# Performance work log

Hardware: AMD Instinct MI355X
Metric: run time of the kernel (lower is better)

## Reference

```python
import jax, jax.numpy as jnp
import numpy as np

TOP_K = 2
EPS = 1e-6

def setup_inputs() -> dict:
    key = jax.random.key(0)
    ks = jax.random.split(key, 6)
    Bt, S, D, E, R = 4, 4096, 1024, 8, 4
    s = lambda d: 1.0 / np.sqrt(d)
    return {
        "x": jax.random.normal(ks[0], (Bt, S, D), jnp.float32),
        "W_base": jax.random.normal(ks[1], (D, D), jnp.float32) * s(D),
        "b_base": jax.random.normal(ks[2], (D,), jnp.float32) * 0.02,
        "W_router": jax.random.normal(ks[3], (E, D), jnp.float32) * s(D),
        "A": jax.random.normal(ks[4], (E, D, R), jnp.float32) * s(D),
        "B": jax.random.normal(ks[5], (E, R, D), jnp.float32) * s(R),
    }

def reference(x, W_base, b_base, W_router, A, B):
    # frozen base linear: [b,s,d] @ [out,d]^T + bias
    base_out = jnp.einsum('bsd,od->bso', x, W_base) + b_base
    # router softmax gate over experts
    logits = jnp.einsum('bsd,ed->bse', x, W_router)
    gate = jax.nn.softmax(logits, axis=-1)
    # top-k scatter-mask (values kept are the gate values themselves)
    topv, topi = jax.lax.top_k(gate, TOP_K)                    # [b,s,k]
    mask = jnp.sum(jax.nn.one_hot(topi, gate.shape[-1], dtype=gate.dtype), axis=-2)
    gate = gate * mask
    gate = gate / (jnp.sum(gate, axis=-1, keepdims=True) + EPS)
    # batched rank-4 LoRA experts, gating applied in low-rank space
    h = jnp.einsum('bsd,edr->bser', x, A)                      # [b,s,E,r]
    hg = h * gate[..., None]                                   # weight before up-proj
    lora_out = jnp.einsum('bser,ero->bso', hg, B)
    return base_out + lora_out
```

## Files before the change

### kernel.cpp

```cpp
#include <hip/hip_runtime.h>
#include <cstdint>

typedef __attribute__((ext_vector_type(8))) short short8;
typedef __attribute__((ext_vector_type(4))) float f32x4;

__device__ inline unsigned short f2bf(float f){
  union { float f; uint32_t u; } v; v.f = f;
  uint32_t r = v.u + 0x7FFFu + ((v.u >> 16) & 1u);
  return (unsigned short)(r >> 16);
}

#define GLL(gp, lp) __builtin_amdgcn_global_load_lds(              \
    (const __attribute__((address_space(1))) void*)(gp),           \
    (__attribute__((address_space(3))) void*)(lp), 16, 0, 0)

__global__ __launch_bounds__(256) void kconv(const float* __restrict__ W,
                                             const float* __restrict__ A,
                                             const float* __restrict__ Bm,
                                             unsigned short* __restrict__ Wb,
                                             unsigned short* __restrict__ BTt,
                                             unsigned short* __restrict__ W2b){
  int i = blockIdx.x * 256 + threadIdx.x;
  Wb[i] = f2bf(W[i]);
  if (i < 32768){
    int o = i >> 5, c = i & 31;
    BTt[i] = f2bf(Bm[(size_t)c*1024 + o]);
    int n = i >> 10, d = i & 1023;
    W2b[i] = f2bf(A[(((size_t)(n>>2))*1024 + d)*4 + (n&3)]);
  }
}

__global__ __launch_bounds__(256) void kxl3(const float* __restrict__ x,
                                            const float* __restrict__ Wr,
                                            unsigned short* __restrict__ xb,
                                            float* __restrict__ gate){
  __shared__ float wr[8192];
  const int tid  = threadIdx.x;
  {
    const float4* s  = (const float4*)Wr;
    float4*       d4 = (float4*)wr;
    #pragma unroll
    for (int j=0;j<8;j++) d4[j*256+tid] = s[j*256+tid];
  }
  __syncthreads();
  const int ln32 = tid & 31;
  const size_t tok = (size_t)blockIdx.x*8 + (tid >> 5);
  const float4* xr = (const float4*)(x + tok*1024);
  ushort4*      xd = (ushort4*)(xb + tok*1024);
  const float4* wv = (const float4*)wr;
  float p[8] = {0.f,0.f,0.f,0.f,0.f,0.f,0.f,0.f};
  #pragma unroll
  for (int c=0;c<8;c++){
    float4 v = xr[c*32 + ln32];
    ushort4 o; o.x=f2bf(v.x); o.y=f2bf(v.y); o.z=f2bf(v.z); o.w=f2bf(v.w);
    xd[c*32 + ln32] = o;
    #pragma unroll
    for (int e=0;e<8;e++){
      float4 wq = wv[e*256 + c*32 + ln32];
      p[e] += v.x*wq.x + v.y*wq.y + v.z*wq.z + v.w*wq.w;
    }
  }
  #pragma unroll
  for (int off=1; off<32; off<<=1){
    #pragma unroll
    for (int e=0;e<8;e++) p[e] += __shfl_xor(p[e], off, 64);
  }
  if (ln32 == 0){
    float mx = p[0];
    #pragma unroll
    for (int e=1;e<8;e++) mx = fmaxf(mx, p[e]);
    float ex[8], s2 = 0.f;
    #pragma unroll
    for (int e=0;e<8;e++){ ex[e] = __expf(p[e]-mx); s2 += ex[e]; }
    int i1 = 0; float v1 = ex[0];
    #pragma unroll
    for (int e=1;e<8;e++) if (ex[e] > v1){ v1 = ex[e]; i1 = e; }
    int i2 = -1; float v2 = -1.f;
    #pragma unroll
    for (int e=0;e<8;e++) if (e != i1 && ex[e] > v2){ v2 = ex[e]; i2 = e; }
    float g1 = v1/s2, g2 = v2/s2;
    float rs = 1.f/(g1 + g2 + 1e-6f);
    float* go = gate + tok*8;
    #pragma unroll
    for (int e=0;e<8;e++) go[e] = (e==i1 ? g1 : (e==i2 ? g2 : 0.f)) * rs;
  }
}

__global__ __launch_bounds__(256) void kh(const unsigned short* __restrict__ xbp,
                                          const unsigned short* __restrict__ W2b,
                                          const float* __restrict__ gate,
                                          unsigned short* __restrict__ HG){
  const int tid  = threadIdx.x;
  const int lane = tid & 63;
  const int wid  = tid >> 6;
  const int lrow = lane & 15;
  const int lk   = (lane >> 4) * 8;
  const int tok0 = blockIdx.x*64 + wid*16;
  f32x4 acc0 = {0.f,0.f,0.f,0.f}, acc1 = {0.f,0.f,0.f,0.f};
  const unsigned short* b0 = W2b + (size_t)lrow*1024 + lk;
  const unsigned short* b1 = W2b + (size_t)(16+lrow)*1024 + lk;
  const unsigned short* ar = xbp + (size_t)(tok0+lrow)*1024 + lk;
  #pragma unroll 4
  for (int ks=0; ks<32; ks++){
    short8 av  = *(const short8*)(ar + ks*32);
    short8 bv0 = *(const short8*)(b0 + ks*32);
    short8 bv1 = *(const short8*)(b1 + ks*32);
    acc0 = __builtin_amdgcn_mfma_f32_16x16x32_bf16(av, bv0, acc0, 0, 0, 0);
    acc1 = __builtin_amdgcn_mfma_f32_16x16x32_bf16(av, bv1, acc1, 0, 0, 0);
  }
  #pragma unroll
  for (int j=0;j<4;j++){
    int tok = tok0 + (lane>>4)*4 + j;
    float g0 = gate[(size_t)tok*8 + (lrow>>2)];
    float g1 = gate[(size_t)tok*8 + 4 + (lrow>>2)];
    HG[(size_t)tok*32 + lrow]      = f2bf(acc0[j]*g0);
    HG[(size_t)tok*32 + 16 + lrow] = f2bf(acc1[j]*g1);
  }
}

__global__ __launch_bounds__(256, 4) void kgemm7(const unsigned short* __restrict__ xb,
                                                 const unsigned short* __restrict__ Wb,
                                                 const unsigned short* __restrict__ BTt,
                                                 const unsigned short* __restrict__ HG,
                                                 const float* __restrict__ bias,
                                                 float* __restrict__ out){
  __shared__ __attribute__((aligned(128))) char lds[32768];
  const int tid  = threadIdx.x;
  const int lane = tid & 63;
  const int w    = tid >> 6;
  const int mblk = blockIdx.x & 127;
  const int nblk = blockIdx.x >> 7;
  const int m0 = mblk << 7, n0 = nblk << 7;
  const int wm = w >> 1, wn = w & 1;
  const int lrow = lane & 15;
  const int q    = lane >> 4;

  const int rowL = lane >> 3;
  const int colb = ((lane & 7) ^ rowL) << 4;
  const int rb   = w * 32;
  const char* Ag = (const char*)xb + ((size_t)(m0 + rb + rowL) << 11) + colb;
  const char* Bg = (const char*)Wb + ((size_t)(n0 + rb + rowL) << 11) + colb;
  char* Ad = lds +         rb*128 + lane*16;
  char* Bd = lds + 16384 + rb*128 + lane*16;

  int offA[4][2], offB[4][2];
  #pragma unroll
  for (int f=0; f<4; f++){
    int ra  = wm*64 + f*16 + lrow;
    int rbn = wn*64 + f*16 + lrow;
    #pragma unroll
    for (int kk=0; kk<2; kk++){
      offA[f][kk] =         ra*128  + ((((kk*4+q) ^ (ra  & 7)) << 4));
      offB[f][kk] = 16384 + rbn*128 + ((((kk*4+q) ^ (rbn & 7)) << 4));
    }
  }

  f32x4 acc[4][4];
  #pragma unroll
  for (int a2=0;a2<4;a2++)
    #pragma unroll
    for (int b2=0;b2<4;b2++) acc[a2][b2] = (f32x4){0.f,0.f,0.f,0.f};

  #pragma unroll 1
  for (int t = 0; t < 16; ++t){
    __syncthreads();
    #pragma unroll
    for (int i=0;i<4;i++) GLL(Ag + (size_t)i*16384 + t*128, Ad + i*1024);
    #pragma unroll
    for (int i=0;i<4;i++) GLL(Bg + (size_t)i*16384 + t*128, Bd + i*1024);
    __syncthreads();
    #pragma unroll
    for (int kk=0; kk<2; kk++){
      short8 a[4], b[4];
      #pragma unroll
      for (int f=0; f<4; f++){
        a[f] = *(const short8*)(lds + offA[f][kk]);
        b[f] = *(const short8*)(lds + offB[f][kk]);
      }
      #pragma unroll
      for (int fm=0;fm<4;fm++)
        #pragma unroll
        for (int fn=0;fn<4;fn++)
          acc[fm][fn] = __builtin_amdgcn_mfma_f32_16x16x32_bf16(a[fm], b[fn], acc[fm][fn], 0, 0, 0);
    }
  }

  {
    short8 ha[4], hb[4];
    #pragma unroll
    for (int f=0; f<4; f++){
      ha[f] = *(const short8*)(HG  + (size_t)(m0 + wm*64 + f*16 + lrow)*32 + q*8);
      hb[f] = *(const short8*)(BTt + (size_t)(n0 + wn*64 + f*16 + lrow)*32 + q*8);
    }
    #pragma unroll
    for (int fm=0;fm<4;fm++)
      #pragma unroll
      for (int fn=0;fn<4;fn++)
        acc[fm][fn] = __builtin_amdgcn_mfma_f32_16x16x32_bf16(ha[fm], hb[fn], acc[fm][fn], 0, 0, 0);
  }

  #pragma unroll
  for (int fn=0;fn<4;fn++){
    int col = n0 + wn*64 + fn*16 + lrow;
    float bv = bias[col];
    #pragma unroll
    for (int fm=0;fm<4;fm++){
      int rbo = m0 + wm*64 + fm*16 + q*4;
      #pragma unroll
      for (int j=0;j<4;j++)
        out[(size_t)(rbo+j)*1024 + col] = acc[fm][fn][j] + bv;
    }
  }
}

extern "C" void kernel_launch(void* const* d_in, const int* in_sizes, int n_in,
                              void* d_out, int out_size, void* d_ws, size_t ws_size,
                              hipStream_t stream){
  const float* x  = (const float*)d_in[0];
  const float* W  = (const float*)d_in[1];
  const float* bb = (const float*)d_in[2];
  const float* Wr = (const float*)d_in[3];
  const float* A  = (const float*)d_in[4];
  const float* Bm = (const float*)d_in[5];
  float* out = (float*)d_out;
  char* ws = (char*)d_ws;

  unsigned short* Wb   = (unsigned short*)(ws + 0);
  unsigned short* BTt  = (unsigned short*)(ws + 2097152);
  unsigned short* W2b  = (unsigned short*)(ws + 2162688);
  float*          gate = (float*)         (ws + 2228224);
  unsigned short* HG   = (unsigned short*)(ws + 2752512);
  unsigned short* xb   = (unsigned short*)(ws + 3801088);

  kconv<<<4096, 256, 0, stream>>>(W, A, Bm, Wb, BTt, W2b);
  kxl3<<<2048, 256, 0, stream>>>(x, Wr, xb, gate);
  kh<<<256, 256, 0, stream>>>(xb, W2b, gate, HG);
  kgemm7<<<1024, 256, 0, stream>>>(xb, Wb, BTt, HG, bb, out);
}
```

Measured before the change: 86.29 us.

## Fuse router logits, bf16 conversion and LoRA down-projection into one kernel

Merges the x-to-bf16 conversion plus router softmax/top-2 kernel with the LoRA down-projection kernel. Each block handles 32 tokens, and its waves split K in halves. The freshly converted x values are shuffled straight into MFMA operands, so x is not re-read from global memory and the gate array round trip disappears. The cost is fewer blocks (512), router weights read from global/L1 instead of LDS, and extra LDS reductions and syncs.

Result: slower. 90.61 us (+5.0%).

```diff
diff --git a/kernel.cpp b/kernel.cpp
--- a/kernel.cpp
+++ b/kernel.cpp
@@ -30,91 +30,119 @@
   }
 }
 
-__global__ __launch_bounds__(256) void kxl3(const float* __restrict__ x,
+__global__ __launch_bounds__(256) void klxh(const float* __restrict__ x,
                                             const float* __restrict__ Wr,
+                                            const unsigned short* __restrict__ W2b,
                                             unsigned short* __restrict__ xb,
-                                            float* __restrict__ gate){
-  __shared__ float wr[8192];
-  const int tid  = threadIdx.x;
-  {
-    const float4* s  = (const float4*)Wr;
-    float4*       d4 = (float4*)wr;
-    #pragma unroll
-    for (int j=0;j<8;j++) d4[j*256+tid] = s[j*256+tid];
-  }
-  __syncthreads();
-  const int ln32 = tid & 31;
-  const size_t tok = (size_t)blockIdx.x*8 + (tid >> 5);
-  const float4* xr = (const float4*)(x + tok*1024);
-  ushort4*      xd = (ushort4*)(xb + tok*1024);
-  const float4* wv = (const float4*)wr;
-  float p[8] = {0.f,0.f,0.f,0.f,0.f,0.f,0.f,0.f};
-  #pragma unroll
-  for (int c=0;c<8;c++){
-    float4 v = xr[c*32 + ln32];
-    ushort4 o; o.x=f2bf(v.x); o.y=f2bf(v.y); o.z=f2bf(v.z); o.w=f2bf(v.w);
-    xd[c*32 + ln32] = o;
-    #pragma unroll
-    for (int e=0;e<8;e++){
-      float4 wq = wv[e*256 + c*32 + ln32];
-      p[e] += v.x*wq.x + v.y*wq.y + v.z*wq.z + v.w*wq.w;
-    }
-  }
-  #pragma unroll
-  for (int off=1; off<32; off<<=1){
-    #pragma unroll
-    for (int e=0;e<8;e++) p[e] += __shfl_xor(p[e], off, 64);
-  }
-  if (ln32 == 0){
-    float mx = p[0];
-    #pragma unroll
-    for (int e=1;e<8;e++) mx = fmaxf(mx, p[e]);
-    float ex[8], s2 = 0.f;
-    #pragma unroll
-    for (int e=0;e<8;e++){ ex[e] = __expf(p[e]-mx); s2 += ex[e]; }
-    int i1 = 0; float v1 = ex[0];
-    #pragma unroll
-    for (int e=1;e<8;e++) if (ex[e] > v1){ v1 = ex[e]; i1 = e; }
-    int i2 = -1; float v2 = -1.f;
-    #pragma unroll
-    for (int e=0;e<8;e++) if (e != i1 && ex[e] > v2){ v2 = ex[e]; i2 = e; }
-    float g1 = v1/s2, g2 = v2/s2;
-    float rs = 1.f/(g1 + g2 + 1e-6f);
-    float* go = gate + tok*8;
-    #pragma unroll
-    for (int e=0;e<8;e++) go[e] = (e==i1 ? g1 : (e==i2 ? g2 : 0.f)) * rs;
-  }
-}
-
-__global__ __launch_bounds__(256) void kh(const unsigned short* __restrict__ xbp,
-                                          const unsigned short* __restrict__ W2b,
-                                          const float* __restrict__ gate,
-                                          unsigned short* __restrict__ HG){
+                                            unsigned short* __restrict__ HG){
+  __shared__ float xch[4][64][8];
+  __shared__ float plog[4][16][8];
+  __shared__ float gl[32][8];
   const int tid  = threadIdx.x;
   const int lane = tid & 63;
   const int wid  = tid >> 6;
+  const int tg   = wid >> 1;
+  const int khf  = wid & 1;
+  const int tok0 = blockIdx.x*32 + tg*16;
+  const int r    = lane >> 2;
+  const int ch   = lane & 3;
   const int lrow = lane & 15;
-  const int lk   = (lane >> 4) * 8;
-  const int tok0 = blockIdx.x*64 + wid*16;
+  const int q8   = lane >> 4;
+  const int srcl = ((lane & 15) << 2) | (lane >> 4);
+
+  const float*    xrow  = x  + (size_t)(tok0 + r)*1024;
+  unsigned short* xbrow = xb + (size_t)(tok0 + r)*1024;
+  const unsigned short* b0p = W2b + (size_t)lrow*1024;
+  const unsigned short* b1p = W2b + (size_t)(16 + lrow)*1024;
+
   f32x4 acc0 = {0.f,0.f,0.f,0.f}, acc1 = {0.f,0.f,0.f,0.f};
-  const unsigned short* b0 = W2b + (size_t)lrow*1024 + lk;
-  const unsigned short* b1 = W2b + (size_t)(16+lrow)*1024 + lk;
-  const unsigned short* ar = xbp + (size_t)(tok0+lrow)*1024 + lk;
-  #pragma unroll 4
-  for (int ks=0; ks<32; ks++){
-    short8 av  = *(const short8*)(ar + ks*32);
-    short8 bv0 = *(const short8*)(b0 + ks*32);
-    short8 bv1 = *(const short8*)(b1 + ks*32);
-    acc0 = __builtin_amdgcn_mfma_f32_16x16x32_bf16(av, bv0, acc0, 0, 0, 0);
-    acc1 = __builtin_amdgcn_mfma_f32_16x16x32_bf16(av, bv1, acc1, 0, 0, 0);
-  }
-  #pragma unroll
-  for (int j=0;j<4;j++){
-    int tok = tok0 + (lane>>4)*4 + j;
-    float g0 = gate[(size_t)tok*8 + (lrow>>2)];
-    float g1 = gate[(size_t)tok*8 + 4 + (lrow>>2)];
-    HG[(size_t)tok*32 + lrow]      = f2bf(acc0[j]*g0);
-    HG[(size_t)tok*32 + 16 + lrow] = f2bf(acc1[j]*g1);
+  float p[8] = {0.f,0.f,0.f,0.f,0.f,0.f,0.f,0.f};
+
+  #pragma unroll 2
+  for (int t=0; t<16; t++){
+    const int k0 = (khf*16 + t)*32 + ch*8;
+    float4 v0 = *(const float4*)(xrow + k0);
+    float4 v1 = *(const float4*)(xrow + k0 + 4);
+    union { short8 s; int i[4]; } cv;
+    cv.i[0] = (int)f2bf(v0.x) | ((int)f2bf(v0.y) << 16);
+    cv.i[1] = (int)f2bf(v0.z) | ((int)f2bf(v0.w) << 16);
+    cv.i[2] = (int)f2bf(v1.x) | ((int)f2bf(v1.y) << 16);
+    cv.i[3] = (int)f2bf(v1.z) | ((int)f2bf(v1.w) << 16);
+    *(int4*)(xbrow + k0) = *(int4*)cv.i;
+    union { short8 s; int i[4]; } av;
+    #pragma unroll
+    for (int u=0; u<4; u++) av.i[u] = __shfl(cv.i[u], srcl, 64);
+    const int kb = (khf*16 + t)*32 + q8*8;
+    short8 bv0 = *(const short8*)(b0p + kb);
+    short8 bv1 = *(const short8*)(b1p + kb);
+    acc0 = __builtin_amdgcn_mfma_f32_16x16x32_bf16(av.s, bv0, acc0, 0, 0, 0);
+    acc1 = __builtin_amdgcn_mfma_f32_16x16x32_bf16(av.s, bv1, acc1, 0, 0, 0);
+    #pragma unroll
+    for (int e=0; e<8; e++){
+      const float* wre = Wr + (size_t)e*1024 + k0;
+      float4 w0 = *(const float4*)(wre);
+      float4 w1 = *(const float4*)(wre + 4);
+      p[e] += v0.x*w0.x + v0.y*w0.y + v0.z*w0.z + v0.w*w0.w
+            + v1.x*w1.x + v1.y*w1.y + v1.z*w1.z + v1.w*w1.w;
+    }
+  }
+
+  #pragma unroll
+  for (int off=1; off<4; off<<=1){
+    #pragma unroll
+    for (int e=0; e<8; e++) p[e] += __shfl_xor(p[e], off, 64);
+  }
+  if (ch == 0){
+    #pragma unroll
+    for (int e=0; e<8; e++) plog[wid][r][e] = p[e];
+  }
+  #pragma unroll
+  for (int j=0; j<4; j++){
+    xch[wid][lane][j]   = acc0[j];
+    xch[wid][lane][4+j] = acc1[j];
+  }
+  __syncthreads();
+
+  if (khf == 0 && lane < 16){
+    float lg[8];
+    #pragma unroll
+    for (int e=0; e<8; e++) lg[e] = plog[wid][lane][e] + plog[wid+1][lane][e];
+    float mx = lg[0];
+    #pragma unroll
+    for (int e=1; e<8; e++) mx = fmaxf(mx, lg[e]);
+    float ex[8], s2 = 0.f;
+    #pragma unroll
+    for (int e=0; e<8; e++){ ex[e] = __expf(lg[e]-mx); s2 += ex[e]; }
+    int i1 = 0; float v1 = ex[0];
+    #pragma unroll
+    for (int e=1; e<8; e++) if (ex[e] > v1){ v1 = ex[e]; i1 = e; }
+    int i2 = -1; float v2 = -1.f;
+    #pragma unroll
+    for (int e=0; e<8; e++) if (e != i1 && ex[e] > v2){ v2 = ex[e]; i2 = e; }
+    float g1 = v1/s2, g2 = v2/s2;
+    float rs = 1.f/(g1 + g2 + 1e-6f);
+    #pragma unroll
+    for (int e=0; e<8; e++)
+      gl[tg*16 + lane][e] = (e==i1 ? g1 : (e==i2 ? g2 : 0.f)) * rs;
+  }
+  __syncthreads();
+
+  if (khf == 0){
+    float h0[4], h1[4];
+    #pragma unroll
+    for (int j=0; j<4; j++){
+      h0[j] = xch[wid][lane][j]   + xch[wid+1][lane][j];
+      h1[j] = xch[wid][lane][4+j] + xch[wid+1][lane][4+j];
+    }
+    #pragma unroll
+    for (int j=0; j<4; j++){
+      int tl = tg*16 + q8*4 + j;
+      size_t tgl = (size_t)blockIdx.x*32 + tl;
+      float g0 = gl[tl][lrow>>2];
+      float g1 = gl[tl][4 + (lrow>>2)];
+      HG[tgl*32 + lrow]      = f2bf(h0[j]*g0);
+      HG[tgl*32 + 16 + lrow] = f2bf(h1[j]*g1);
+    }
   }
 }
 
@@ -228,12 +256,10 @@
   unsigned short* Wb   = (unsigned short*)(ws + 0);
   unsigned short* BTt  = (unsigned short*)(ws + 2097152);
   unsigned short* W2b  = (unsigned short*)(ws + 2162688);
-  float*          gate = (float*)         (ws + 2228224);
-  unsigned short* HG   = (unsigned short*)(ws + 2752512);
-  unsigned short* xb   = (unsigned short*)(ws + 3801088);
+  unsigned short* HG   = (unsigned short*)(ws + 2228224);
+  unsigned short* xb   = (unsigned short*)(ws + 3276800);
 
   kconv<<<4096, 256, 0, stream>>>(W, A, Bm, Wb, BTt, W2b);
-  kxl3<<<2048, 256, 0, stream>>>(x, Wr, xb, gate);
-  kh<<<256, 256, 0, stream>>>(xb, W2b, gate, HG);
+  klxh<<<512, 256, 0, stream>>>(x, Wr, W2b, xb, HG);
   kgemm7<<<1024, 256, 0, stream>>>(xb, Wb, BTt, HG, bb, out);
 }
```

## Fuse weight conversion into x/router kernel and split-K the LoRA down-projection

Applied to the files above, without the earlier changes.

The standalone weight-conversion kernel is folded into the x-to-bf16 and router kernel, with each thread converting two W elements and the small B/A transposes, which removes one launch and its tail. The low-rank projection kernel now uses 1024 blocks of 128 threads and splits K across two waves, combining the halves through LDS, so more of the GPU works on this small kernel. The cost is extra LDS traffic and a barrier, plus a larger, more register-heavy fused kernel.

Result: slower. 94.46 us (+9.5%).

```diff
diff --git a/kernel.cpp b/kernel.cpp
--- a/kernel.cpp
+++ b/kernel.cpp
@@ -14,26 +14,16 @@
     (const __attribute__((address_space(1))) void*)(gp),           \
     (__attribute__((address_space(3))) void*)(lp), 16, 0, 0)
 
-__global__ __launch_bounds__(256) void kconv(const float* __restrict__ W,
-                                             const float* __restrict__ A,
-                                             const float* __restrict__ Bm,
-                                             unsigned short* __restrict__ Wb,
-                                             unsigned short* __restrict__ BTt,
-                                             unsigned short* __restrict__ W2b){
-  int i = blockIdx.x * 256 + threadIdx.x;
-  Wb[i] = f2bf(W[i]);
-  if (i < 32768){
-    int o = i >> 5, c = i & 31;
-    BTt[i] = f2bf(Bm[(size_t)c*1024 + o]);
-    int n = i >> 10, d = i & 1023;
-    W2b[i] = f2bf(A[(((size_t)(n>>2))*1024 + d)*4 + (n&3)]);
-  }
-}
-
-__global__ __launch_bounds__(256) void kxl3(const float* __restrict__ x,
+__global__ __launch_bounds__(256) void kxl4(const float* __restrict__ x,
                                             const float* __restrict__ Wr,
+                                            const float* __restrict__ W,
+                                            const float* __restrict__ A,
+                                            const float* __restrict__ Bm,
                                             unsigned short* __restrict__ xb,
-                                            float* __restrict__ gate){
+                                            float* __restrict__ gate,
+                                            unsigned short* __restrict__ Wb,
+                                            unsigned short* __restrict__ BTt,
+                                            unsigned short* __restrict__ W2b){
   __shared__ float wr[8192];
   const int tid  = threadIdx.x;
   {
@@ -60,6 +50,22 @@
       p[e] += v.x*wq.x + v.y*wq.y + v.z*wq.z + v.w*wq.w;
     }
   }
+  {
+    const size_t i0 = ((size_t)blockIdx.x*256 + tid)*2;
+    float2 wv2 = *(const float2*)(W + i0);
+    unsigned int pk = (unsigned)f2bf(wv2.x) | ((unsigned)f2bf(wv2.y) << 16);
+    *(unsigned int*)(Wb + i0) = pk;
+    if (i0 < 32768){
+      #pragma unroll
+      for (int u=0; u<2; u++){
+        size_t i = i0 + u;
+        int o = (int)(i >> 5), c = (int)(i & 31);
+        BTt[i] = f2bf(Bm[(size_t)c*1024 + o]);
+        int n = (int)(i >> 10), d = (int)(i & 1023);
+        W2b[i] = f2bf(A[(((size_t)(n>>2))*1024 + d)*4 + (n&3)]);
+      }
+    }
+  }
   #pragma unroll
   for (int off=1; off<32; off<<=1){
     #pragma unroll
@@ -86,35 +92,45 @@
   }
 }
 
-__global__ __launch_bounds__(256) void kh(const unsigned short* __restrict__ xbp,
-                                          const unsigned short* __restrict__ W2b,
-                                          const float* __restrict__ gate,
-                                          unsigned short* __restrict__ HG){
+__global__ __launch_bounds__(128) void kh2(const unsigned short* __restrict__ xbp,
+                                           const unsigned short* __restrict__ W2b,
+                                           const float* __restrict__ gate,
+                                           unsigned short* __restrict__ HG){
+  __shared__ float red[64][8];
   const int tid  = threadIdx.x;
   const int lane = tid & 63;
-  const int wid  = tid >> 6;
+  const int kh   = tid >> 6;
   const int lrow = lane & 15;
   const int lk   = (lane >> 4) * 8;
-  const int tok0 = blockIdx.x*64 + wid*16;
+  const int tok0 = blockIdx.x*16;
   f32x4 acc0 = {0.f,0.f,0.f,0.f}, acc1 = {0.f,0.f,0.f,0.f};
-  const unsigned short* b0 = W2b + (size_t)lrow*1024 + lk;
-  const unsigned short* b1 = W2b + (size_t)(16+lrow)*1024 + lk;
-  const unsigned short* ar = xbp + (size_t)(tok0+lrow)*1024 + lk;
+  const unsigned short* b0 = W2b + (size_t)lrow*1024      + kh*512 + lk;
+  const unsigned short* b1 = W2b + (size_t)(16+lrow)*1024 + kh*512 + lk;
+  const unsigned short* ar = xbp + (size_t)(tok0+lrow)*1024 + kh*512 + lk;
   #pragma unroll 4
-  for (int ks=0; ks<32; ks++){
+  for (int ks=0; ks<16; ks++){
     short8 av  = *(const short8*)(ar + ks*32);
     short8 bv0 = *(const short8*)(b0 + ks*32);
     short8 bv1 = *(const short8*)(b1 + ks*32);
     acc0 = __builtin_amdgcn_mfma_f32_16x16x32_bf16(av, bv0, acc0, 0, 0, 0);
     acc1 = __builtin_amdgcn_mfma_f32_16x16x32_bf16(av, bv1, acc1, 0, 0, 0);
   }
-  #pragma unroll
-  for (int j=0;j<4;j++){
-    int tok = tok0 + (lane>>4)*4 + j;
-    float g0 = gate[(size_t)tok*8 + (lrow>>2)];
-    float g1 = gate[(size_t)tok*8 + 4 + (lrow>>2)];
-    HG[(size_t)tok*32 + lrow]      = f2bf(acc0[j]*g0);
-    HG[(size_t)tok*32 + 16 + lrow] = f2bf(acc1[j]*g1);
+  if (kh == 1){
+    #pragma unroll
+    for (int j=0;j<4;j++){ red[lane][j] = acc0[j]; red[lane][4+j] = acc1[j]; }
+  }
+  __syncthreads();
+  if (kh == 0){
+    #pragma unroll
+    for (int j=0;j<4;j++){
+      int tok = tok0 + (lane>>4)*4 + j;
+      float h0 = acc0[j] + red[lane][j];
+      float h1 = acc1[j] + red[lane][4+j];
+      float g0 = gate[(size_t)tok*8 + (lrow>>2)];
+      float g1 = gate[(size_t)tok*8 + 4 + (lrow>>2)];
+      HG[(size_t)tok*32 + lrow]      = f2bf(h0*g0);
+      HG[(size_t)tok*32 + 16 + lrow] = f2bf(h1*g1);
+    }
   }
 }
 
@@ -232,8 +248,7 @@
   unsigned short* HG   = (unsigned short*)(ws + 2752512);
   unsigned short* xb   = (unsigned short*)(ws + 3801088);
 
-  kconv<<<4096, 256, 0, stream>>>(W, A, Bm, Wb, BTt, W2b);
-  kxl3<<<2048, 256, 0, stream>>>(x, Wr, xb, gate);
-  kh<<<256, 256, 0, stream>>>(xb, W2b, gate, HG);
+  kxl4<<<2048, 256, 0, stream>>>(x, Wr, W, A, Bm, xb, gate, Wb, BTt, W2b);
+  kh2<<<1024, 128, 0, stream>>>(xb, W2b, gate, HG);
   kgemm7<<<1024, 256, 0, stream>>>(xb, Wb, BTt, HG, bb, out);
 }
```
